# Kernel tuning notes

Hardware: AMD Instinct MI355X
Metric: run time of the kernel (lower is better)

## Reference

```python
import jax, jax.numpy as jnp
import numpy as np

N_NODES = 50000
N_EDGES = 600000
IN_CH = 128
HID = 256
OUT_FEAT = 256
OUT_CH = 128
EPS = 1e-12


def _sage_conv(x, src, dst, mask_f, Wl, bl, Wr, n_nodes):
    # PyG SAGEConv: out = lin_l(mean_{j in N(i)} x_j) + lin_r(x_i); L2-normalize rows.
    msg = x[src] * mask_f[:, None]                                  # [E, d] gather
    agg = jax.ops.segment_sum(msg, dst, num_segments=n_nodes)      # [N, d]
    cnt = jax.ops.segment_sum(mask_f, dst, num_segments=n_nodes)   # [N]
    agg = agg / jnp.maximum(cnt, 1.0)[:, None]                      # mean over kept edges
    out = agg @ Wl.T + bl + x @ Wr.T                                 # [N, h]
    nrm = jnp.maximum(jnp.linalg.norm(out, axis=-1, keepdims=True), EPS)
    return out / nrm


def setup_inputs() -> dict:
    key = jax.random.key(0)
    ks = jax.random.split(key, 12)
    x = jax.random.normal(ks[0], (N_NODES, IN_CH), dtype=jnp.float32)
    edge_index = jax.random.randint(ks[1], (2, N_EDGES), 0, N_NODES, dtype=jnp.int32)
    edge_mask = jax.random.bernoulli(ks[2], 0.7, (N_EDGES,))  # dropout_edge p=0.3 keep mask

    def lin(k, fan_out, fan_in):
        s = 1.0 / np.sqrt(fan_in)
        return jax.random.uniform(k, (fan_out, fan_in), jnp.float32, -s, s)

    W1l = lin(ks[3], HID, IN_CH)
    b1 = jnp.zeros((HID,), jnp.float32)
    W1r = lin(ks[4], HID, IN_CH)
    Ws = lin(ks[5], HID, IN_CH)
    bs = jnp.zeros((HID,), jnp.float32)
    W2l = lin(ks[6], OUT_FEAT, HID)
    b2 = jnp.zeros((OUT_FEAT,), jnp.float32)
    W2r = lin(ks[7], OUT_FEAT, HID)
    Wo = lin(ks[8], OUT_CH, OUT_FEAT)
    bo = jnp.zeros((OUT_CH,), jnp.float32)
    return {"x": x, "edge_index": edge_index, "edge_mask": edge_mask,
            "W1l": W1l, "b1": b1, "W1r": W1r, "Ws": Ws, "bs": bs,
            "W2l": W2l, "b2": b2, "W2r": W2r, "Wo": Wo, "bo": bo}


def reference(x, edge_index, edge_mask, W1l, b1, W1r, Ws, bs, W2l, b2, W2r, Wo, bo):
    src, dst = edge_index[0], edge_index[1]
    ones = jnp.ones((src.shape[0],), x.dtype)
    # conv1 uses all edges
    h = _sage_conv(x, src, dst, ones, W1l, b1, W1r, N_NODES)
    h = h + (x @ Ws.T + bs)
    h = jnp.tanh(h)
    # conv2 uses edge-dropped graph (mask = kept edges)
    mask_f = edge_mask.astype(x.dtype)
    h = jnp.tanh(_sage_conv(h, src, dst, mask_f, W2l, b2, W2r, N_NODES))
    return h @ Wo.T + bo
```

## Files before the change

### kernel.cpp

```cpp
#include <hip/hip_runtime.h>
#include <hip/hip_bf16.h>

#define N_NODES 50000
#define N_PAD   50048
#define N_EDGES 600000
#define IN_CH 128
#define HID 256
#define OUT_CH 128

typedef unsigned short u16;
typedef unsigned char u8;
typedef unsigned int u32;

typedef __attribute__((ext_vector_type(8))) short short8;
typedef __attribute__((ext_vector_type(4))) float f32x4;

typedef __attribute__((address_space(3))) u32 as3_u32;
typedef __attribute__((address_space(1))) const u32 as1_u32;

__device__ __forceinline__ float bf2f(u16 v) {
    unsigned u = ((unsigned)v) << 16;
    return __uint_as_float(u);
}
__device__ __forceinline__ u16 f2bf(float f) {
    unsigned u = __float_as_uint(f);
    u += 0x7FFF + ((u >> 16) & 1);
    return (u16)(u >> 16);
}

__device__ __forceinline__ void async16(const void* g, void* l) {
    __builtin_amdgcn_global_load_lds((as1_u32*)g, (as3_u32*)l, 16, 0, 0);
}

__global__ void detect_kernel(const u16* __restrict__ xu, const u8* __restrict__ mb,
                              int* __restrict__ flags) {
    int lane = threadIdx.x & 63;

    int inr = 0;
    {
        u32 w0 = ((const u32*)xu)[lane * 2 + 0];
        u32 w1 = ((const u32*)xu)[lane * 2 + 1];
        u16 h[4] = {(u16)w0, (u16)(w0 >> 16), (u16)w1, (u16)(w1 >> 16)};
#pragma unroll
        for (int j = 0; j < 4; j++) {
            int e = (h[j] >> 7) & 0xFF;
            if (e >= 100 && e <= 133) inr++;
        }
    }

    int c1 = 0, c23 = 0, h3f_1 = 0, h3f_3 = 0;
#pragma unroll
    for (int t = 0; t < 16; t++) {
        u32 w = ((const u32*)mb)[t * 64 + lane];
        u8 b1 = (u8)(w >> 8), b2 = (u8)(w >> 16), b3 = (u8)(w >> 24);
        if (b1) c1++;
        if (b1 == 0x3F) h3f_1 = 1;
        if (b2) c23++;
        if (b3) c23++;
        if (b3 == 0x3F) h3f_3 = 1;
    }

#pragma unroll
    for (int off = 32; off > 0; off >>= 1) {
        inr   += __shfl_xor(inr, off, 64);
        c1    += __shfl_xor(c1, off, 64);
        c23   += __shfl_xor(c23, off, 64);
        h3f_1 |= __shfl_xor(h3f_1, off, 64);
        h3f_3 |= __shfl_xor(h3f_3, off, 64);
    }

    if (lane == 0 && blockIdx.x == 0) {
        flags[0] = (inr >= 200) ? 1 : 0;
        int fmt;
        if (h3f_1) fmt = 3;
        else if (h3f_3) fmt = 2;
        else if (c1 + c23 > 0) fmt = 0;
        else fmt = 1;
        flags[1] = fmt;
    }
}

#define NX (N_NODES * IN_CH)
__global__ void convert_all_kernel(const void* __restrict__ x,
                                   const void* __restrict__ W1l, const void* __restrict__ W1r,
                                   const void* __restrict__ Ws,
                                   const void* __restrict__ W2l, const void* __restrict__ W2r,
                                   const void* __restrict__ Wo,
                                   const void* __restrict__ b1, const void* __restrict__ bs,
                                   const void* __restrict__ b2, const void* __restrict__ bo,
                                   u16* __restrict__ xb, u16* __restrict__ Wc1,
                                   u16* __restrict__ Wsb, u16* __restrict__ Wc2,
                                   u16* __restrict__ Wob, float* __restrict__ biasf,
                                   const int* __restrict__ flags) {
    int i = blockIdx.x * blockDim.x + threadIdx.x;
    int isbf = flags[0];
    auto cv = [&](const void* s, int idx) -> u16 {
        return isbf ? ((const u16*)s)[idx] : f2bf(((const float*)s)[idx]);
    };
    if (i < NX) { xb[i] = cv(x, i); return; }
    i -= NX;
    if (i < 256 * 256) {
        int n = i >> 8, k = i & 255;
        const void* s = (k < 128) ? W1l : W1r;
        Wc1[i] = cv(s, n * 128 + (k & 127));
        return;
    }
    i -= 256 * 256;
    if (i < 256 * 128) { Wsb[i] = cv(Ws, i); return; }
    i -= 256 * 128;
    if (i < 256 * 512) {
        int n = i >> 9, k = i & 511;
        const void* s = (k < 256) ? W2l : W2r;
        Wc2[i] = cv(s, n * 256 + (k & 255));
        return;
    }
    i -= 256 * 512;
    if (i < 128 * 256) { Wob[i] = cv(Wo, i); return; }
    i -= 128 * 256;
    if (i < 896) {
        const void* s; int idx;
        if (i < 256)      { s = b1; idx = i; }
        else if (i < 512) { s = bs; idx = i - 256; }
        else if (i < 768) { s = b2; idx = i - 512; }
        else              { s = bo; idx = i - 768; }
        biasf[i] = isbf ? bf2f(((const u16*)s)[idx]) : ((const float*)s)[idx];
    }
}
#define CONV_TOTAL (NX + 256 * 256 + 256 * 128 + 256 * 512 + 128 * 256 + 896)

__global__ void hist_kernel(const int* __restrict__ ei, const void* __restrict__ em,
                            u32* __restrict__ degp, u32* __restrict__ rankp,
                            const int* __restrict__ flags) {
    int i = blockIdx.x * blockDim.x + threadIdx.x;
    if (i >= N_EDGES) return;
    int d = ei[N_EDGES + i];
    int fmt = flags[1];
    bool keep;
    if (fmt == 0)      keep = ((const u8*)em)[i] != 0;
    else if (fmt == 1) keep = ((const int*)em)[i] != 0;
    else if (fmt == 2) keep = ((const float*)em)[i] != 0.f;
    else               keep = ((const u16*)em)[i] != 0;
    u32 inc = keep ? 0x10001u : 1u;
    u32 old = atomicAdd(&degp[d], inc);
    rankp[i] = (old & 0xffffu) | (keep ? (old & 0xffff0000u) : 0xffff0000u);
}

__global__ void partial_kernel(const u32* __restrict__ degp, u32* __restrict__ partial) {
    __shared__ u32 sh[256];
    int t = threadIdx.x;
    int i = blockIdx.x * 256 + t;
    sh[t] = (i < N_NODES) ? degp[i] : 0;
    __syncthreads();
    for (int s = 128; s > 0; s >>= 1) {
        if (t < s) sh[t] += sh[t + s];
        __syncthreads();
    }
    if (t == 0) partial[blockIdx.x] = sh[0];
}

__global__ void scanp_kernel(const u32* __restrict__ partial, int* __restrict__ pscan, int nb) {
    __shared__ int sh[256];
    int t = threadIdx.x;
    u32 pv = (t < nb) ? partial[t] : 0;
    int v1 = pv & 0xffff, v2 = pv >> 16;
    sh[t] = v1;
    __syncthreads();
    for (int o = 1; o < 256; o <<= 1) {
        int u = (t >= o) ? sh[t - o] : 0;
        __syncthreads();
        sh[t] += u;
        __syncthreads();
    }
    if (t < nb) pscan[t] = sh[t] - v1;
    __syncthreads();
    sh[t] = v2;
    __syncthreads();
    for (int o = 1; o < 256; o <<= 1) {
        int u = (t >= o) ? sh[t - o] : 0;
        __syncthreads();
        sh[t] += u;
        __syncthreads();
    }
    if (t < nb) pscan[nb + t] = sh[t] - v2;
}

__global__ void rowptr_kernel(const u32* __restrict__ degp, const int* __restrict__ pscan,
                              int* __restrict__ row_ptr, int* __restrict__ row_ptr2, int nb) {
    __shared__ u32 sh[256];
    int t = threadIdx.x;
    int i = blockIdx.x * 256 + t;
    u32 v = (i < N_NODES) ? degp[i] : 0;
    sh[t] = v;
    __syncthreads();
    for (int o = 1; o < 256; o <<= 1) {
        u32 u = (t >= o) ? sh[t - o] : 0;
        __syncthreads();
        sh[t] += u;
        __syncthreads();
    }
    u32 ex = sh[t] - v;
    if (i <= N_NODES) {
        row_ptr[i]  = pscan[blockIdx.x] + (int)(ex & 0xffff);
        row_ptr2[i] = pscan[nb + blockIdx.x] + (int)(ex >> 16);
    }
}

__global__ void scatter_csr_kernel(const int* __restrict__ ei, const u32* __restrict__ rankp,
                                   const int* __restrict__ row_ptr, const int* __restrict__ row_ptr2,
                                   int* __restrict__ srcs, int* __restrict__ srcs2) {
    int i = blockIdx.x * blockDim.x + threadIdx.x;
    if (i >= N_EDGES) return;
    int d = ei[N_EDGES + i];
    int s = ei[i];
    u32 rp = rankp[i];
    srcs[row_ptr[d] + (int)(rp & 0xffffu)] = s;
    u32 kr = rp >> 16;
    if (kr != 0xffffu) srcs2[row_ptr2[d] + (int)kr] = s;
}

__global__ __launch_bounds__(256) void gather1_kernel(const int* __restrict__ row_ptr,
                                                      const int* __restrict__ srcs,
                                                      const u16* __restrict__ xb,
                                                      u16* __restrict__ aggb) {
    int wid = (blockIdx.x * blockDim.x + threadIdx.x) >> 6;
    int lane = threadIdx.x & 63;
    if (wid >= N_NODES) return;
    int start = row_ptr[wid], end = row_ptr[wid + 1];
    int dg = end - start;
    int sv = (lane < dg) ? srcs[start + lane] : 0;
    float a0 = 0.f, a1 = 0.f, b0 = 0.f, b1 = 0.f;
    float c0 = 0.f, c1 = 0.f, d0 = 0.f, d1 = 0.f;
    int n = dg < 64 ? dg : 64;
    int e = 0;
    for (; e + 4 <= n; e += 4) {
        int s0 = __builtin_amdgcn_readlane(sv, e);
        int s1 = __builtin_amdgcn_readlane(sv, e + 1);
        int s2 = __builtin_amdgcn_readlane(sv, e + 2);
        int s3 = __builtin_amdgcn_readlane(sv, e + 3);
        u32 v0 = *(const u32*)(xb + (size_t)s0 * IN_CH + lane * 2);
        u32 v1 = *(const u32*)(xb + (size_t)s1 * IN_CH + lane * 2);
        u32 v2 = *(const u32*)(xb + (size_t)s2 * IN_CH + lane * 2);
        u32 v3 = *(const u32*)(xb + (size_t)s3 * IN_CH + lane * 2);
        a0 += bf2f((u16)v0); a1 += bf2f((u16)(v0 >> 16));
        b0 += bf2f((u16)v1); b1 += bf2f((u16)(v1 >> 16));
        c0 += bf2f((u16)v2); c1 += bf2f((u16)(v2 >> 16));
        d0 += bf2f((u16)v3); d1 += bf2f((u16)(v3 >> 16));
    }
    for (; e < n; e++) {
        int s0 = __builtin_amdgcn_readlane(sv, e);
        u32 v0 = *(const u32*)(xb + (size_t)s0 * IN_CH + lane * 2);
        a0 += bf2f((u16)v0); a1 += bf2f((u16)(v0 >> 16));
    }
    for (e = 64; e < dg; e++) {
        int s0 = srcs[start + e];
        u32 v0 = *(const u32*)(xb + (size_t)s0 * IN_CH + lane * 2);
        a0 += bf2f((u16)v0); a1 += bf2f((u16)(v0 >> 16));
    }
    float inv = 1.f / fmaxf((float)dg, 1.f);
    float rx = (a0 + b0) + (c0 + d0);
    float ry = (a1 + b1) + (c1 + d1);
    u32 o = (u32)f2bf(rx * inv) | ((u32)f2bf(ry * inv) << 16);
    *(u32*)(aggb + (size_t)wid * IN_CH + lane * 2) = o;
}

__global__ __launch_bounds__(256) void gather2_kernel(const int* __restrict__ row_ptr2,
                                                      const int* __restrict__ srcs2,
                                                      const u16* __restrict__ h1b,
                                                      u16* __restrict__ aggb) {
    int wid = (blockIdx.x * blockDim.x + threadIdx.x) >> 6;
    int lane = threadIdx.x & 63;
    if (wid >= N_NODES) return;
    int start = row_ptr2[wid], end = row_ptr2[wid + 1];
    int dg = end - start;
    int sv = (lane < dg) ? srcs2[start + lane] : 0;
    float a0 = 0.f, a1 = 0.f, a2 = 0.f, a3 = 0.f;
    float b0 = 0.f, b1 = 0.f, b2 = 0.f, b3 = 0.f;
    float c0 = 0.f, c1 = 0.f, c2 = 0.f, c3 = 0.f;
    float d0 = 0.f, d1 = 0.f, d2 = 0.f, d3 = 0.f;
    int n = dg < 64 ? dg : 64;
    int e = 0;
    for (; e + 4 <= n; e += 4) {
        int s0 = __builtin_amdgcn_readlane(sv, e);
        int s1 = __builtin_amdgcn_readlane(sv, e + 1);
        int s2 = __builtin_amdgcn_readlane(sv, e + 2);
        int s3 = __builtin_amdgcn_readlane(sv, e + 3);
        uint2 v = *(const uint2*)(h1b + (size_t)s0 * HID + lane * 4);
        uint2 w = *(const uint2*)(h1b + (size_t)s1 * HID + lane * 4);
        uint2 y = *(const uint2*)(h1b + (size_t)s2 * HID + lane * 4);
        uint2 zz = *(const uint2*)(h1b + (size_t)s3 * HID + lane * 4);
        a0 += bf2f((u16)v.x); a1 += bf2f((u16)(v.x >> 16));
        a2 += bf2f((u16)v.y); a3 += bf2f((u16)(v.y >> 16));
        b0 += bf2f((u16)w.x); b1 += bf2f((u16)(w.x >> 16));
        b2 += bf2f((u16)w.y); b3 += bf2f((u16)(w.y >> 16));
        c0 += bf2f((u16)y.x); c1 += bf2f((u16)(y.x >> 16));
        c2 += bf2f((u16)y.y); c3 += bf2f((u16)(y.y >> 16));
        d0 += bf2f((u16)zz.x); d1 += bf2f((u16)(zz.x >> 16));
        d2 += bf2f((u16)zz.y); d3 += bf2f((u16)(zz.y >> 16));
    }
    for (; e < n; e++) {
        int s0 = __builtin_amdgcn_readlane(sv, e);
        uint2 v = *(const uint2*)(h1b + (size_t)s0 * HID + lane * 4);
        a0 += bf2f((u16)v.x); a1 += bf2f((u16)(v.x >> 16));
        a2 += bf2f((u16)v.y); a3 += bf2f((u16)(v.y >> 16));
    }
    for (e = 64; e < dg; e++) {
        int s0 = srcs2[start + e];
        uint2 v = *(const uint2*)(h1b + (size_t)s0 * HID + lane * 4);
        a0 += bf2f((u16)v.x); a1 += bf2f((u16)(v.x >> 16));
        a2 += bf2f((u16)v.y); a3 += bf2f((u16)(v.y >> 16));
    }
    float inv = 1.f / fmaxf((float)dg, 1.f);
    float r0 = (a0 + b0) + (c0 + d0);
    float r1 = (a1 + b1) + (c1 + d1);
    float r2 = (a2 + b2) + (c2 + d2);
    float r3 = (a3 + b3) + (c3 + d3);
    u32 o0 = (u32)f2bf(r0 * inv) | ((u32)f2bf(r1 * inv) << 16);
    u32 o1 = (u32)f2bf(r2 * inv) | ((u32)f2bf(r3 * inv) << 16);
    u16* p = aggb + (size_t)wid * HID + lane * 4;
    *(u32*)p = o0;
    *(u32*)(p + 2) = o1;
}

template<int MODE>
__global__ __launch_bounds__(256, 2) void gemm_staged(
    const u16* __restrict__ A0, const u16* __restrict__ A1,
    const u16* __restrict__ W0, const u16* __restrict__ W1,
    const float* __restrict__ bias0, const float* __restrict__ bias1,
    u16* __restrict__ outb, void* __restrict__ outv, const int* __restrict__ flags) {

    constexpr int NT  = (MODE == 3) ? 2 : 4;
    constexpr int Nw  = NT * 16;
    constexpr int NKS = (MODE == 1) ? 6 : ((MODE == 2) ? 8 : 4);
    constexpr int BBYTES = NT * 64 * 128;
    __shared__ __align__(16) u8 ldsmem[16384 + 2 * BBYTES];

    int tid = threadIdx.x;
    int w = tid >> 6, lane = tid & 63;
    int q = lane >> 4, c = lane & 15;
    int m_base = blockIdx.x * 64;
    int rj = lane >> 3, jj = lane & 7;
    int j16 = ((jj ^ rj) << 4);

    f32x4 acc[4][NT], acc2[4][NT];
    const f32x4 z = {0.f, 0.f, 0.f, 0.f};
#pragma unroll
    for (int mt = 0; mt < 4; mt++)
#pragma unroll
        for (int nt = 0; nt < NT; nt++) { acc[mt][nt] = z; acc2[mt][nt] = z; }

    auto stage = [&](int ks, int b) {
        const u16* ap; int astr, kta;
        const u16* wp; int wstr, ktw;
        if (MODE == 1) {
            astr = 128;
            if (ks < 2)      { ap = A0; kta = ks; }
            else if (ks < 4) { ap = A1; kta = ks - 2; }
            else             { ap = A1; kta = ks - 4; }
            if (ks < 4) { wp = W0; wstr = 256; ktw = ks; }
            else        { wp = W1; wstr = 128; ktw = ks - 4; }
        } else if (MODE == 2) {
            astr = 256;
            if (ks < 4) { ap = A0; kta = ks; } else { ap = A1; kta = ks - 4; }
            wp = W0; wstr = 512; ktw = ks;
        } else {
            astr = 256; ap = A0; kta = ks;
            wp = W0; wstr = 256; ktw = ks;
        }
#pragma unroll
        for (int t = 0; t < 2; t++) {
            int r = w * 16 + t * 8;
            const u8* g = (const u8*)(ap + (size_t)(m_base + r + rj) * astr) + kta * 128 + j16;
            async16(g, ldsmem + b * 8192 + r * 128);
        }
#pragma unroll
        for (int t = 0; t < NT * 2; t++) {
            int n = w * Nw + t * 8;
            const u8* g = (const u8*)(wp + (size_t)(n + rj) * wstr) + ktw * 128 + j16;
            async16(g, ldsmem + 16384 + b * BBYTES + n * 128);
        }
    };

    auto compute = [&](int b, f32x4 (*tgt)[NT]) {
        const u8* ab = ldsmem + b * 8192;
        const u8* bb = ldsmem + 16384 + b * BBYTES;
#pragma unroll
        for (int kk = 0; kk < 2; kk++) {
            int sA = (((kk * 4 + q) ^ (c & 7)) << 4);
            short8 af[4], bfr[NT];
#pragma unroll
            for (int mt = 0; mt < 4; mt++)
                af[mt] = *(const short8*)(ab + (mt * 16 + c) * 128 + sA);
#pragma unroll
            for (int nt = 0; nt < NT; nt++)
                bfr[nt] = *(const short8*)(bb + (w * Nw + nt * 16 + c) * 128 + sA);
#pragma unroll
            for (int mt = 0; mt < 4; mt++)
#pragma unroll
                for (int nt = 0; nt < NT; nt++)
                    tgt[mt][nt] = __builtin_amdgcn_mfma_f32_16x16x32_bf16(af[mt], bfr[nt], tgt[mt][nt], 0, 0, 0);
        }
    };

    stage(0, 0);
    int b = 0;
#pragma unroll
    for (int ks = 0; ks < NKS; ks++) {
        __syncthreads();
        if (ks + 1 < NKS) stage(ks + 1, b ^ 1);
        if (MODE == 1 && ks >= 4) compute(b, acc2);
        else                      compute(b, acc);
        b ^= 1;
    }
    __syncthreads();

    if (MODE == 3) {
        float bcol[NT];
#pragma unroll
        for (int nt = 0; nt < NT; nt++) bcol[nt] = bias0[w * Nw + nt * 16 + c];
        int isbf = flags[0];
#pragma unroll
        for (int mt = 0; mt < 4; mt++)
#pragma unroll
            for (int r = 0; r < 4; r++) {
                int row = m_base + mt * 16 + q * 4 + r;
                if (row < N_NODES) {
#pragma unroll
                    for (int nt = 0; nt < NT; nt++) {
                        float v = acc[mt][nt][r] + bcol[nt];
                        int col = w * Nw + nt * 16 + c;
                        if (isbf) ((u16*)outv)[(size_t)row * OUT_CH + col] = f2bf(v);
                        else      ((float*)outv)[(size_t)row * OUT_CH + col] = v;
                    }
                }
            }
    } else {
        float* redf = (float*)ldsmem;
        float bcol[NT], b2col[NT];
#pragma unroll
        for (int nt = 0; nt < NT; nt++) {
            int col = w * Nw + nt * 16 + c;
            bcol[nt] = bias0[col];
            if (MODE == 1) b2col[nt] = bias1[col];
        }
        float s[4][4];
#pragma unroll
        for (int mt = 0; mt < 4; mt++)
#pragma unroll
            for (int r = 0; r < 4; r++) {
                float t = 0.f;
#pragma unroll
                for (int nt = 0; nt < NT; nt++) {
                    float v = acc[mt][nt][r] + bcol[nt];
                    acc[mt][nt][r] = v;
                    t += v * v;
                }
                s[mt][r] = t;
            }
#pragma unroll
        for (int off = 1; off < 16; off <<= 1) {
#pragma unroll
            for (int mt = 0; mt < 4; mt++)
#pragma unroll
                for (int r = 0; r < 4; r++)
                    s[mt][r] += __shfl_xor(s[mt][r], off, 64);
        }
        if (c == 0) {
#pragma unroll
            for (int mt = 0; mt < 4; mt++)
#pragma unroll
                for (int r = 0; r < 4; r++)
                    redf[(mt * 16 + q * 4 + r) * 4 + w] = s[mt][r];
        }
        __syncthreads();
        if (tid < 64) {
            float t = redf[tid * 4] + redf[tid * 4 + 1] + redf[tid * 4 + 2] + redf[tid * 4 + 3];
            redf[256 + tid] = 1.f / fmaxf(sqrtf(t), 1e-12f);
        }
        __syncthreads();
#pragma unroll
        for (int mt = 0; mt < 4; mt++)
#pragma unroll
            for (int r = 0; r < 4; r++) {
                int rl = mt * 16 + q * 4 + r;
                int row = m_base + rl;
                if (row < N_NODES) {
                    float iv = redf[256 + rl];
#pragma unroll
                    for (int nt = 0; nt < NT; nt++) {
                        int col = w * Nw + nt * 16 + c;
                        float h;
                        if (MODE == 1) h = acc[mt][nt][r] * iv + acc2[mt][nt][r] + b2col[nt];
                        else           h = acc[mt][nt][r] * iv;
                        outb[(size_t)row * HID + col] = f2bf(tanhf(h));
                    }
                }
            }
    }
}

extern "C" void kernel_launch(void* const* d_in, const int* in_sizes, int n_in,
                              void* d_out, int out_size, void* d_ws, size_t ws_size,
                              hipStream_t stream) {
    const void* x    = d_in[0];
    const int*  ei   = (const int*)d_in[1];
    const void* em   = d_in[2];
    const void* W1l  = d_in[3];
    const void* b1   = d_in[4];
    const void* W1r  = d_in[5];
    const void* Ws   = d_in[6];
    const void* bs   = d_in[7];
    const void* W2l  = d_in[8];
    const void* b2   = d_in[9];
    const void* W2r  = d_in[10];
    const void* Wo   = d_in[11];
    const void* bo   = d_in[12];

    char* p = (char*)d_ws;
    auto carve = [&](size_t bytes) { char* r = p; p += (bytes + 63) & ~(size_t)63; return r; };
    int*   flags   = (int*)carve(256);
    u16*   xb      = (u16*)carve((size_t)N_PAD * IN_CH * 2);
    u16*   h1b     = (u16*)carve((size_t)N_PAD * HID * 2);
    u16*   aggb    = (u16*)carve((size_t)N_PAD * HID * 2);
    u16*   h2b     = (u16*)carve((size_t)N_PAD * HID * 2);
    u16*   Wc1     = (u16*)carve(256 * 256 * 2);
    u16*   Wsb     = (u16*)carve(256 * 128 * 2);
    u16*   Wc2     = (u16*)carve(256 * 512 * 2);
    u16*   Wob     = (u16*)carve(128 * 256 * 2);
    float* biasf   = (float*)carve(896 * 4);
    u32*   degp    = (u32*)carve(50176 * 4);
    int*   row_ptr = (int*)carve(50056 * 4);
    int*   row_ptr2= (int*)carve(50056 * 4);
    u32*   partial = (u32*)carve(256 * 4);
    int*   pscan   = (int*)carve(512 * 4);
    u32*   rankp   = (u32*)carve((size_t)N_EDGES * 4);
    int*   srcs    = (int*)carve((size_t)N_EDGES * 4);
    int*   srcs2   = (int*)carve((size_t)N_EDGES * 4);
    float* b1f = biasf, *bsf = biasf + 256, *b2f = biasf + 512, *bof = biasf + 768;
    (void)ws_size; (void)in_sizes; (void)n_in; (void)out_size;

    detect_kernel<<<1, 64, 0, stream>>>((const u16*)x, (const u8*)em, flags);

    convert_all_kernel<<<(CONV_TOTAL + 255) / 256, 256, 0, stream>>>(
        x, W1l, W1r, Ws, W2l, W2r, Wo, b1, bs, b2, bo,
        xb, Wc1, Wsb, Wc2, Wob, biasf, flags);

    hipMemsetAsync(degp, 0, 50176 * sizeof(u32), stream);
    hist_kernel<<<(N_EDGES + 255) / 256, 256, 0, stream>>>(ei, em, degp, rankp, flags);
    const int NB = (N_NODES + 255) / 256;
    partial_kernel<<<NB, 256, 0, stream>>>(degp, partial);
    scanp_kernel<<<1, 256, 0, stream>>>(partial, pscan, NB);
    rowptr_kernel<<<NB, 256, 0, stream>>>(degp, pscan, row_ptr, row_ptr2, NB);
    scatter_csr_kernel<<<(N_EDGES + 255) / 256, 256, 0, stream>>>(ei, rankp, row_ptr, row_ptr2, srcs, srcs2);

    const int GB = N_PAD / 64;

    gather1_kernel<<<(N_NODES * 64) / 256, 256, 0, stream>>>(row_ptr, srcs, xb, aggb);
    gemm_staged<1><<<GB, 256, 0, stream>>>(aggb, xb, Wc1, Wsb, b1f, bsf, h1b, nullptr, flags);

    gather2_kernel<<<(N_NODES * 64) / 256, 256, 0, stream>>>(row_ptr2, srcs2, h1b, aggb);
    gemm_staged<2><<<GB, 256, 0, stream>>>(aggb, h1b, Wc2, nullptr, b2f, nullptr, h2b, nullptr, flags);

    gemm_staged<3><<<GB, 256, 0, stream>>>(h2b, nullptr, Wob, nullptr, bof, nullptr, nullptr, d_out, flags);
}
```

Measured before the change: 306.3 us.

## Fuse output linear into conv2 GEMM epilogue and fold degree memset into convert

The final output projection is fused into the conv2 GEMM epilogue. The tanh-normalized hidden tile is written to LDS in bf16, and Wo is staged in two halves and multiplied with MFMA, so the h2 intermediate never goes to global memory and one launch is removed. The degree-array memset moves into the conversion kernel, tanhf is replaced by an exp2/rcp approximation, and bf16 stores are paired via lane shuffles. The costs are more LDS traffic and synchronization in the epilogue, plus slightly lower precision in tanh.

```diff
diff --git a/kernel.cpp b/kernel.cpp
--- a/kernel.cpp
+++ b/kernel.cpp
@@ -26,6 +26,11 @@
     unsigned u = __float_as_uint(f);
     u += 0x7FFF + ((u >> 16) & 1);
     return (u16)(u >> 16);
+}
+
+__device__ __forceinline__ float fast_tanh(float x) {
+    float e = __builtin_amdgcn_exp2f(x * 2.88539008177793f);
+    return 1.f - 2.f * __builtin_amdgcn_rcpf(e + 1.f);
 }
 
 __device__ __forceinline__ void async16(const void* g, void* l) {
@@ -81,6 +86,7 @@
 }
 
 #define NX (N_NODES * IN_CH)
+#define DEGP_N 50176
 __global__ void convert_all_kernel(const void* __restrict__ x,
                                    const void* __restrict__ W1l, const void* __restrict__ W1r,
                                    const void* __restrict__ Ws,
@@ -91,6 +97,7 @@
                                    u16* __restrict__ xb, u16* __restrict__ Wc1,
                                    u16* __restrict__ Wsb, u16* __restrict__ Wc2,
                                    u16* __restrict__ Wob, float* __restrict__ biasf,
+                                   u32* __restrict__ degp,
                                    const int* __restrict__ flags) {
     int i = blockIdx.x * blockDim.x + threadIdx.x;
     int isbf = flags[0];
@@ -124,9 +131,12 @@
         else if (i < 768) { s = b2; idx = i - 512; }
         else              { s = bo; idx = i - 768; }
         biasf[i] = isbf ? bf2f(((const u16*)s)[idx]) : ((const float*)s)[idx];
-    }
-}
-#define CONV_TOTAL (NX + 256 * 256 + 256 * 128 + 256 * 512 + 128 * 256 + 896)
+        return;
+    }
+    i -= 896;
+    if (i < DEGP_N) degp[i] = 0;
+}
+#define CONV_TOTAL (NX + 256 * 256 + 256 * 128 + 256 * 512 + 128 * 256 + 896 + DEGP_N)
 
 __global__ void hist_kernel(const int* __restrict__ ei, const void* __restrict__ em,
                             u32* __restrict__ degp, u32* __restrict__ rankp,
@@ -328,9 +338,9 @@
     const float* __restrict__ bias0, const float* __restrict__ bias1,
     u16* __restrict__ outb, void* __restrict__ outv, const int* __restrict__ flags) {
 
-    constexpr int NT  = (MODE == 3) ? 2 : 4;
+    constexpr int NT  = 4;
     constexpr int Nw  = NT * 16;
-    constexpr int NKS = (MODE == 1) ? 6 : ((MODE == 2) ? 8 : 4);
+    constexpr int NKS = (MODE == 1) ? 6 : 8;
     constexpr int BBYTES = NT * 64 * 128;
     __shared__ __align__(16) u8 ldsmem[16384 + 2 * BBYTES];
 
@@ -358,13 +368,10 @@
             else             { ap = A1; kta = ks - 4; }
             if (ks < 4) { wp = W0; wstr = 256; ktw = ks; }
             else        { wp = W1; wstr = 128; ktw = ks - 4; }
-        } else if (MODE == 2) {
+        } else {
             astr = 256;
             if (ks < 4) { ap = A0; kta = ks; } else { ap = A1; kta = ks - 4; }
             wp = W0; wstr = 512; ktw = ks;
-        } else {
-            astr = 256; ap = A0; kta = ks;
-            wp = W0; wstr = 256; ktw = ks;
         }
 #pragma unroll
         for (int t = 0; t < 2; t++) {
@@ -413,70 +420,50 @@
     }
     __syncthreads();
 
-    if (MODE == 3) {
-        float bcol[NT];
-#pragma unroll
-        for (int nt = 0; nt < NT; nt++) bcol[nt] = bias0[w * Nw + nt * 16 + c];
-        int isbf = flags[0];
+    float* redf = (float*)ldsmem;
+    float bcol[NT];
+#pragma unroll
+    for (int nt = 0; nt < NT; nt++) bcol[nt] = bias0[w * Nw + nt * 16 + c];
+    float s[4][4];
+#pragma unroll
+    for (int mt = 0; mt < 4; mt++)
+#pragma unroll
+        for (int r = 0; r < 4; r++) {
+            float t = 0.f;
+#pragma unroll
+            for (int nt = 0; nt < NT; nt++) {
+                float v = acc[mt][nt][r] + bcol[nt];
+                acc[mt][nt][r] = v;
+                t += v * v;
+            }
+            s[mt][r] = t;
+        }
+#pragma unroll
+    for (int off = 1; off < 16; off <<= 1) {
 #pragma unroll
         for (int mt = 0; mt < 4; mt++)
 #pragma unroll
-            for (int r = 0; r < 4; r++) {
-                int row = m_base + mt * 16 + q * 4 + r;
-                if (row < N_NODES) {
-#pragma unroll
-                    for (int nt = 0; nt < NT; nt++) {
-                        float v = acc[mt][nt][r] + bcol[nt];
-                        int col = w * Nw + nt * 16 + c;
-                        if (isbf) ((u16*)outv)[(size_t)row * OUT_CH + col] = f2bf(v);
-                        else      ((float*)outv)[(size_t)row * OUT_CH + col] = v;
-                    }
-                }
-            }
-    } else {
-        float* redf = (float*)ldsmem;
-        float bcol[NT], b2col[NT];
-#pragma unroll
-        for (int nt = 0; nt < NT; nt++) {
-            int col = w * Nw + nt * 16 + c;
-            bcol[nt] = bias0[col];
-            if (MODE == 1) b2col[nt] = bias1[col];
-        }
-        float s[4][4];
+            for (int r = 0; r < 4; r++)
+                s[mt][r] += __shfl_xor(s[mt][r], off, 64);
+    }
+    if (c == 0) {
 #pragma unroll
         for (int mt = 0; mt < 4; mt++)
 #pragma unroll
-            for (int r = 0; r < 4; r++) {
-                float t = 0.f;
-#pragma unroll
-                for (int nt = 0; nt < NT; nt++) {
-                    float v = acc[mt][nt][r] + bcol[nt];
-                    acc[mt][nt][r] = v;
-                    t += v * v;
-                }
-                s[mt][r] = t;
-            }
-#pragma unroll
-        for (int off = 1; off < 16; off <<= 1) {
-#pragma unroll
-            for (int mt = 0; mt < 4; mt++)
-#pragma unroll
-                for (int r = 0; r < 4; r++)
-                    s[mt][r] += __shfl_xor(s[mt][r], off, 64);
-        }
-        if (c == 0) {
-#pragma unroll
-            for (int mt = 0; mt < 4; mt++)
-#pragma unroll
-                for (int r = 0; r < 4; r++)
-                    redf[(mt * 16 + q * 4 + r) * 4 + w] = s[mt][r];
-        }
-        __syncthreads();
-        if (tid < 64) {
-            float t = redf[tid * 4] + redf[tid * 4 + 1] + redf[tid * 4 + 2] + redf[tid * 4 + 3];
-            redf[256 + tid] = 1.f / fmaxf(sqrtf(t), 1e-12f);
-        }
-        __syncthreads();
+            for (int r = 0; r < 4; r++)
+                redf[(mt * 16 + q * 4 + r) * 4 + w] = s[mt][r];
+    }
+    __syncthreads();
+    if (tid < 64) {
+        float t = redf[tid * 4] + redf[tid * 4 + 1] + redf[tid * 4 + 2] + redf[tid * 4 + 3];
+        redf[256 + tid] = 1.f / fmaxf(sqrtf(t), 1e-12f);
+    }
+    __syncthreads();
+
+    if (MODE == 1) {
+        float b2col[NT];
+#pragma unroll
+        for (int nt = 0; nt < NT; nt++) b2col[nt] = bias1[w * Nw + nt * 16 + c];
 #pragma unroll
         for (int mt = 0; mt < 4; mt++)
 #pragma unroll
@@ -488,13 +475,100 @@
 #pragma unroll
                     for (int nt = 0; nt < NT; nt++) {
                         int col = w * Nw + nt * 16 + c;
-                        float h;
-                        if (MODE == 1) h = acc[mt][nt][r] * iv + acc2[mt][nt][r] + b2col[nt];
-                        else           h = acc[mt][nt][r] * iv;
-                        outb[(size_t)row * HID + col] = f2bf(tanhf(h));
+                        float t = fast_tanh(acc[mt][nt][r] * iv + acc2[mt][nt][r] + b2col[nt]);
+                        float tp = __shfl_xor(t, 1, 64);
+                        if (!(lane & 1)) {
+                            u32 pk = (u32)f2bf(t) | ((u32)f2bf(tp) << 16);
+                            *(u32*)(outb + (size_t)row * HID + col) = pk;
+                        }
                     }
                 }
             }
+    } else {
+        u8* h2l = ldsmem + 16384;
+        u8* wol = ldsmem + 16384 + BBYTES;
+        int rj2 = lane >> 5, s5 = lane & 31;
+
+        auto stageWo = [&](int half) {
+#pragma unroll
+            for (int t = 0; t < 8; t++) {
+                int rl = w * 16 + t * 2 + rj2;
+                const u8* g = (const u8*)W1 + (((size_t)(half * 64 + rl)) << 9)
+                            + ((s5 ^ (rl & 7)) << 4);
+                async16(g, wol + (w * 16 + t * 2) * 512);
+            }
+        };
+
+        stageWo(0);
+#pragma unroll
+        for (int mt = 0; mt < 4; mt++)
+#pragma unroll
+            for (int r = 0; r < 4; r++) {
+                int rl = mt * 16 + q * 4 + r;
+                float iv = redf[256 + rl];
+#pragma unroll
+                for (int nt = 0; nt < NT; nt++) {
+                    int k = w * Nw + nt * 16 + c;
+                    float t = fast_tanh(acc[mt][nt][r] * iv);
+                    float tp = __shfl_xor(t, 1, 64);
+                    if (!(lane & 1)) {
+                        u32 pk = (u32)f2bf(t) | ((u32)f2bf(tp) << 16);
+                        int off = rl * 512 + ((((k >> 3) ^ (rl & 7)) << 4)) + ((k & 7) << 1);
+                        *(u32*)(h2l + off) = pk;
+                    }
+                }
+            }
+        __syncthreads();
+
+        int isbf = flags[0];
+        float bO0 = bias1[w * 16 + c];
+        float bO1 = bias1[64 + w * 16 + c];
+
+        auto computeO = [&](f32x4* accO) {
+#pragma unroll
+            for (int kk = 0; kk < 8; kk++) {
+                int sw = (((kk * 4 + q) ^ (c & 7)) << 4);
+                short8 bfO = *(const short8*)(wol + (w * 16 + c) * 512 + sw);
+#pragma unroll
+                for (int mt = 0; mt < 4; mt++) {
+                    short8 afO = *(const short8*)(h2l + (mt * 16 + c) * 512 + sw);
+                    accO[mt] = __builtin_amdgcn_mfma_f32_16x16x32_bf16(afO, bfO, accO[mt], 0, 0, 0);
+                }
+            }
+        };
+        auto storeO = [&](int half, float bO, f32x4* accO) {
+#pragma unroll
+            for (int mt = 0; mt < 4; mt++)
+#pragma unroll
+                for (int r = 0; r < 4; r++) {
+                    int row = m_base + mt * 16 + q * 4 + r;
+                    if (row < N_NODES) {
+                        int col = half * 64 + w * 16 + c;
+                        float v = accO[mt][r] + bO;
+                        if (isbf) {
+                            float vp = __shfl_xor(v, 1, 64);
+                            if (!(lane & 1))
+                                *(u32*)((u16*)outv + (size_t)row * OUT_CH + col) =
+                                    (u32)f2bf(v) | ((u32)f2bf(vp) << 16);
+                        } else {
+                            ((float*)outv)[(size_t)row * OUT_CH + col] = v;
+                        }
+                    }
+                }
+        };
+
+        f32x4 accO[4];
+#pragma unroll
+        for (int mt = 0; mt < 4; mt++) accO[mt] = z;
+        computeO(accO);
+        __syncthreads();
+        stageWo(1);
+        storeO(0, bO0, accO);
+        __syncthreads();
+#pragma unroll
+        for (int mt = 0; mt < 4; mt++) accO[mt] = z;
+        computeO(accO);
+        storeO(1, bO1, accO);
     }
 }
 
@@ -521,7 +595,6 @@
     u16*   xb      = (u16*)carve((size_t)N_PAD * IN_CH * 2);
     u16*   h1b     = (u16*)carve((size_t)N_PAD * HID * 2);
     u16*   aggb    = (u16*)carve((size_t)N_PAD * HID * 2);
-    u16*   h2b     = (u16*)carve((size_t)N_PAD * HID * 2);
     u16*   Wc1     = (u16*)carve(256 * 256 * 2);
     u16*   Wsb     = (u16*)carve(256 * 128 * 2);
     u16*   Wc2     = (u16*)carve(256 * 512 * 2);
@@ -542,9 +615,8 @@
 
     convert_all_kernel<<<(CONV_TOTAL + 255) / 256, 256, 0, stream>>>(
         x, W1l, W1r, Ws, W2l, W2r, Wo, b1, bs, b2, bo,
-        xb, Wc1, Wsb, Wc2, Wob, biasf, flags);
-
-    hipMemsetAsync(degp, 0, 50176 * sizeof(u32), stream);
+        xb, Wc1, Wsb, Wc2, Wob, biasf, degp, flags);
+
     hist_kernel<<<(N_EDGES + 255) / 256, 256, 0, stream>>>(ei, em, degp, rankp, flags);
     const int NB = (N_NODES + 255) / 256;
     partial_kernel<<<NB, 256, 0, stream>>>(degp, partial);
@@ -558,7 +630,5 @@
     gemm_staged<1><<<GB, 256, 0, stream>>>(aggb, xb, Wc1, Wsb, b1f, bsf, h1b, nullptr, flags);
 
     gather2_kernel<<<(N_NODES * 64) / 256, 256, 0, stream>>>(row_ptr2, srcs2, h1b, aggb);
-    gemm_staged<2><<<GB, 256, 0, stream>>>(aggb, h1b, Wc2, nullptr, b2f, nullptr, h2b, nullptr, flags);
-
-    gemm_staged<3><<<GB, 256, 0, stream>>>(h2b, nullptr, Wob, nullptr, bof, nullptr, nullptr, d_out, flags);
-}
+    gemm_staged<2><<<GB, 256, 0, stream>>>(aggb, h1b, Wc2, Wob, b2f, bof, nullptr, d_out, flags);
+}
```

Measured after the change: 295.3 us, median of 2. 3.6% less time.
